# Optimization experiments

Hardware: AMD Instinct MI355X
Metric: run time of the kernel (lower is better)

The kernel has to match this reference:

```python
import jax, jax.numpy as jnp
import numpy as np
from functools import partial

SEQ, BATCH, IN, HID = 512, 128, 256, 1024


def setup_inputs() -> dict:
    key = jax.random.key(0)
    ks = jax.random.split(key, 8)
    std = 1.0 / np.sqrt(HID)
    u = lambda k, shape: jax.random.uniform(k, shape, jnp.float32, -std, std)
    return {
        "inp": jax.random.normal(ks[0], (SEQ, BATCH, IN), jnp.float32),
        "Wxh": u(ks[1], (4 * HID, IN)),
        "bxh": u(ks[2], (4 * HID,)),
        "Whh": u(ks[3], (4 * HID, HID)),
        "bhh": u(ks[4], (4 * HID,)),
        "Wout": u(ks[5], (IN, HID)),
        "bout": u(ks[6], (IN,)),
    }


def lstm_forward(inp, Wxh, bxh, Whh, bhh, Wout, bout):
    seq, batch, _ = inp.shape
    hid = Whh.shape[1]
    # Precompute input projection for all timesteps: [T, B, 4H]
    x_proj = jnp.einsum("tbi,gi->tbg", inp, Wxh) + bxh

    def step(carry, xp_t):
        h, c = carry
        gates = xp_t + h @ Whh.T + bhh            # [B, 4H]
        i, f, g, o = jnp.split(gates, 4, axis=-1)  # torch chunk order: i,f,g,o
        c = jax.nn.sigmoid(f) * c + jax.nn.sigmoid(i) * jnp.tanh(g)
        h = jax.nn.sigmoid(o) * jnp.tanh(c)
        return (h, c), h

    h0 = jnp.zeros((batch, hid), inp.dtype)
    c0 = jnp.zeros((batch, hid), inp.dtype)
    _, hs = jax.lax.scan(step, (h0, c0), x_proj)   # hs: [T, B, H]
    out = jnp.einsum("tbh,ih->tbi", hs, Wout) + bout
    return jax.nn.log_softmax(out, axis=-1)


def reference(inp, Wxh, bxh, Whh, bhh, Wout, bout):
    return lstm_forward(inp, Wxh, bxh, Whh, bhh, Wout, bout)
```

## Files before the change

### kernel.cpp

```cpp
#include <hip/hip_runtime.h>
#include <math.h>


#define TT  512
#define BB  128
#define NIN 256
#define NH  1024
#define G4  4096
#define KK  1280

typedef __bf16 bf16_t;
typedef bf16_t bf16x8 __attribute__((ext_vector_type(8)));
typedef float  f32x4  __attribute__((ext_vector_type(4)));


__global__ void conv_w_kernel(const float* __restrict__ Wxh,
                              const float* __restrict__ Whh,
                              bf16_t* __restrict__ Wc) {
  const int n = blockIdx.y;
  const int k = blockIdx.x * 256 + threadIdx.x;
  const int g = n & 3, j = n >> 2;
  float v = (k < NIN) ? Wxh[(size_t)(g * NH + j) * NIN + k]
                      : Whh[(size_t)(g * NH + j) * NH + (k - NIN)];
  Wc[(size_t)n * KK + k] = (bf16_t)v;
}

__global__ void conv_f2b_kernel(const float* __restrict__ src,
                                bf16_t* __restrict__ dst, int n4) {
  int i = blockIdx.x * 256 + threadIdx.x;
  if (i < n4) {
    float4 v = ((const float4*)src)[i];
    dst[i * 4 + 0] = (bf16_t)v.x;
    dst[i * 4 + 1] = (bf16_t)v.y;
    dst[i * 4 + 2] = (bf16_t)v.z;
    dst[i * 4 + 3] = (bf16_t)v.w;
  }
}

__global__ void prep_bias_kernel(const float* __restrict__ bxh,
                                 const float* __restrict__ bhh,
                                 float* __restrict__ bsum4) {
  int n = blockIdx.x * 256 + threadIdx.x;
  int g = n & 3, j = n >> 2;
  bsum4[n] = bxh[g * NH + j] + bhh[g * NH + j];
}


__global__ __launch_bounds__(256) void fused_step(
    int t,
    const bf16_t* __restrict__ x_bf,
    const bf16_t* __restrict__ Wc,
    const float*  __restrict__ bsum4,
    const bf16_t* __restrict__ h_cur,
    bf16_t*       __restrict__ h_next,
    float*        __restrict__ c,
    const bf16_t* __restrict__ WoutB,
    const float*  __restrict__ bout,
    float*        __restrict__ logits_w,
    const float*  __restrict__ logits_r,
    float*        __restrict__ out)
{
  const int blk  = blockIdx.x;
  const int tid  = threadIdx.x;
  const int lane = tid & 63;
  const int wv   = tid >> 6;
  const int l16  = lane & 15;
  const int lq   = lane >> 4;

  if (blk < 256) {
    if (t >= TT) return;
    __shared__ float gs[32][68];
    const int bm = (blk & 3) * 32;
    const int bn = (blk >> 2) * 64;
    const int wm = wv & 1, wn = wv >> 1;
    const int m0 = bm + wm * 16;
    const int n0 = bn + wn * 32;

    const bf16_t* ax  = x_bf + (size_t)t * BB * NIN + (size_t)(m0 + l16) * NIN + lq * 8;
    const bf16_t* ah  = h_cur + (size_t)(m0 + l16) * NH + lq * 8;
    const bf16_t* b0p = Wc + (size_t)(n0 + l16) * KK + lq * 8;
    const bf16_t* b1p = Wc + (size_t)(n0 + 16 + l16) * KK + lq * 8;

    f32x4 acc0 = {0.f, 0.f, 0.f, 0.f};
    f32x4 acc1 = {0.f, 0.f, 0.f, 0.f};

#pragma unroll 4
    for (int kk = 0; kk < NIN; kk += 32) {
      bf16x8 a  = *(const bf16x8*)(ax + kk);
      bf16x8 b0 = *(const bf16x8*)(b0p + kk);
      bf16x8 b1 = *(const bf16x8*)(b1p + kk);
      acc0 = __builtin_amdgcn_mfma_f32_16x16x32_bf16(a, b0, acc0, 0, 0, 0);
      acc1 = __builtin_amdgcn_mfma_f32_16x16x32_bf16(a, b1, acc1, 0, 0, 0);
    }
#pragma unroll 4
    for (int kk = 0; kk < NH; kk += 32) {
      bf16x8 a  = *(const bf16x8*)(ah + kk);
      bf16x8 b0 = *(const bf16x8*)(b0p + NIN + kk);
      bf16x8 b1 = *(const bf16x8*)(b1p + NIN + kk);
      acc0 = __builtin_amdgcn_mfma_f32_16x16x32_bf16(a, b0, acc0, 0, 0, 0);
      acc1 = __builtin_amdgcn_mfma_f32_16x16x32_bf16(a, b1, acc1, 0, 0, 0);
    }

#pragma unroll
    for (int r = 0; r < 4; ++r) {
      gs[wm * 16 + lq * 4 + r][wn * 32 + l16]      = acc0[r];
      gs[wm * 16 + lq * 4 + r][wn * 32 + 16 + l16] = acc1[r];
    }
    __syncthreads();

#pragma unroll
    for (int p = 0; p < 2; ++p) {
      const int u  = tid + p * 256;
      const int bl = u >> 4, jl = u & 15;
      float4 g4 = *(const float4*)&gs[bl][jl * 4];
      const int jg = (bn >> 2) + jl;
      float4 bs = ((const float4*)bsum4)[jg];
      const float gi = g4.x + bs.x;
      const float gf = g4.y + bs.y;
      const float gg = g4.z + bs.z;
      const float go = g4.w + bs.w;
      const float si = 1.f / (1.f + __expf(-gi));
      const float sf = 1.f / (1.f + __expf(-gf));
      const float so = 1.f / (1.f + __expf(-go));
      const float tg = tanhf(gg);
      const size_t idx = (size_t)(bm + bl) * NH + jg;
      const float cn = sf * c[idx] + si * tg;
      c[idx] = cn;
      h_next[idx] = (bf16_t)(so * tanhf(cn));
    }
  } else if (blk < 288) {
    if (t < 1 || t > TT) return;
    const int b2 = blk - 256;
    const int m0 = (b2 >> 2) * 16;
    const int n0 = (b2 & 3) * 64 + wv * 16;

    const bf16_t* ap = h_cur + (size_t)(m0 + l16) * NH + lq * 8;
    const bf16_t* bp = WoutB + (size_t)(n0 + l16) * NH + lq * 8;
    f32x4 acc = {0.f, 0.f, 0.f, 0.f};
#pragma unroll 4
    for (int kk = 0; kk < NH; kk += 32) {
      bf16x8 a = *(const bf16x8*)(ap + kk);
      bf16x8 b = *(const bf16x8*)(bp + kk);
      acc = __builtin_amdgcn_mfma_f32_16x16x32_bf16(a, b, acc, 0, 0, 0);
    }
    const int col = n0 + l16;
    const float bo = bout[col];
#pragma unroll
    for (int r = 0; r < 4; ++r)
      logits_w[(size_t)(m0 + lq * 4 + r) * NIN + col] = acc[r] + bo;
  } else {
    if (t < 2) return;
    __shared__ float red[2][4][4];
    const int b0 = (blk - 288) * 4;
    const float* lb = logits_r + (size_t)b0 * NIN;
    float v[4], mx[4], sm[4];
#pragma unroll
    for (int r = 0; r < 4; ++r) v[r] = lb[r * NIN + tid];
#pragma unroll
    for (int r = 0; r < 4; ++r) mx[r] = v[r];
#pragma unroll
    for (int off = 32; off > 0; off >>= 1)
#pragma unroll
      for (int r = 0; r < 4; ++r) mx[r] = fmaxf(mx[r], __shfl_xor(mx[r], off));
    if (lane == 0)
#pragma unroll
      for (int r = 0; r < 4; ++r) red[0][wv][r] = mx[r];
    __syncthreads();
#pragma unroll
    for (int r = 0; r < 4; ++r)
      mx[r] = fmaxf(fmaxf(red[0][0][r], red[0][1][r]),
                    fmaxf(red[0][2][r], red[0][3][r]));
#pragma unroll
    for (int r = 0; r < 4; ++r) sm[r] = __expf(v[r] - mx[r]);
#pragma unroll
    for (int off = 32; off > 0; off >>= 1)
#pragma unroll
      for (int r = 0; r < 4; ++r) sm[r] += __shfl_xor(sm[r], off);
    if (lane == 0)
#pragma unroll
      for (int r = 0; r < 4; ++r) red[1][wv][r] = sm[r];
    __syncthreads();
    float* ot = out + (size_t)(t - 2) * BB * NIN + (size_t)b0 * NIN;
#pragma unroll
    for (int r = 0; r < 4; ++r) {
      float S = red[1][0][r] + red[1][1][r] + red[1][2][r] + red[1][3][r];
      ot[r * NIN + tid] = v[r] - mx[r] - logf(S);
    }
  }
}


extern "C" void kernel_launch(void* const* d_in, const int* in_sizes, int n_in,
                              void* d_out, int out_size, void* d_ws, size_t ws_size,
                              hipStream_t stream) {
  const float* inp  = (const float*)d_in[0];
  const float* Wxh  = (const float*)d_in[1];
  const float* bxh  = (const float*)d_in[2];
  const float* Whh  = (const float*)d_in[3];
  const float* bhh  = (const float*)d_in[4];
  const float* Wout = (const float*)d_in[5];
  const float* bout = (const float*)d_in[6];
  float* out = (float*)d_out;

  char* p = (char*)d_ws;
  bf16_t* Wc    = (bf16_t*)p; p += (size_t)G4 * KK * 2;
  bf16_t* x_bf  = (bf16_t*)p; p += (size_t)TT * BB * NIN * 2;
  bf16_t* WoutB = (bf16_t*)p; p += (size_t)NIN * NH * 2;
  bf16_t* h0    = (bf16_t*)p; p += (size_t)BB * NH * 2;
  bf16_t* h1    = (bf16_t*)p; p += (size_t)BB * NH * 2;
  float*  cbuf  = (float*)p;  p += (size_t)BB * NH * 4;
  float*  bsum4 = (float*)p;  p += (size_t)G4 * 4;
  float*  lg0   = (float*)p;  p += (size_t)BB * NIN * 4;
  float*  lg1   = (float*)p;  p += (size_t)BB * NIN * 4;

  conv_w_kernel<<<dim3(KK / 256, G4), 256, 0, stream>>>(Wxh, Whh, Wc);
  conv_f2b_kernel<<<(TT * BB * NIN / 4 + 255) / 256, 256, 0, stream>>>(
      inp, x_bf, TT * BB * NIN / 4);
  conv_f2b_kernel<<<(NIN * NH / 4 + 255) / 256, 256, 0, stream>>>(
      Wout, WoutB, NIN * NH / 4);
  prep_bias_kernel<<<G4 / 256, 256, 0, stream>>>(bxh, bhh, bsum4);
  hipMemsetAsync(h0, 0, (size_t)BB * NH * 2, stream);
  hipMemsetAsync(cbuf, 0, (size_t)BB * NH * 4, stream);

  bf16_t* hb[2] = {h0, h1};
  float*  lg[2] = {lg0, lg1};
  for (int t = 0; t < TT + 2; ++t) {
    fused_step<<<320, 256, 0, stream>>>(
        t, x_bf, Wc, bsum4,
        hb[t & 1], hb[(t + 1) & 1], cbuf,
        WoutB, bout,
        lg[t & 1],
        lg[(t + 1) & 1],
        out);
  }
}
```

Measured before the change: 12.59 ms.

## Replace per-timestep launches with persistent cooperative kernel holding weights in registers

The 514 per-step kernel launches become one cooperative persistent kernel of 256 blocks that loops over timesteps and separates them with grid.sync(). Each wave loads its slice of the combined input and recurrent weights into 40 registers of bf16x8 once and reuses it for every step, so those weights are no longer re-read from memory each step. The cell state moves from a global buffer into per-thread registers. The costs are a grid-wide barrier per step, high register pressure from the resident weights, and the requirement that all 256 blocks be co-resident at once.

```diff
diff --git a/kernel.cpp b/kernel.cpp
--- a/kernel.cpp
+++ b/kernel.cpp
@@ -1,6 +1,9 @@
 #include <hip/hip_runtime.h>
+#include <hip/hip_cooperative_groups.h>
 #include <math.h>
 
+
+namespace cg = cooperative_groups;
 
 #define TT  512
 #define BB  128
@@ -12,6 +15,8 @@
 typedef __bf16 bf16_t;
 typedef bf16_t bf16x8 __attribute__((ext_vector_type(8)));
 typedef float  f32x4  __attribute__((ext_vector_type(4)));
+
+#define MFMA(a, b, c) __builtin_amdgcn_mfma_f32_16x16x32_bf16((a), (b), (c), 0, 0, 0)
 
 
 __global__ void conv_w_kernel(const float* __restrict__ Wxh,
@@ -46,20 +51,22 @@
 }
 
 
-__global__ __launch_bounds__(256) void fused_step(
-    int t,
+__global__ __launch_bounds__(256, 1) void lstm_persistent(
     const bf16_t* __restrict__ x_bf,
     const bf16_t* __restrict__ Wc,
     const float*  __restrict__ bsum4,
-    const bf16_t* __restrict__ h_cur,
-    bf16_t*       __restrict__ h_next,
-    float*        __restrict__ c,
+    bf16_t* __restrict__ hb0,
+    bf16_t* __restrict__ hb1,
+    float*  __restrict__ lgA,
+    float*  __restrict__ lgB,
     const bf16_t* __restrict__ WoutB,
     const float*  __restrict__ bout,
-    float*        __restrict__ logits_w,
-    const float*  __restrict__ logits_r,
-    float*        __restrict__ out)
+    float*  __restrict__ out)
 {
+  cg::grid_group grid = cg::this_grid();
+  __shared__ float gs[64 * 40];
+  __shared__ float red[2][4][4];
+
   const int blk  = blockIdx.x;
   const int tid  = threadIdx.x;
   const int lane = tid & 63;
@@ -67,125 +74,151 @@
   const int l16  = lane & 15;
   const int lq   = lane >> 4;
 
-  if (blk < 256) {
-    if (t >= TT) return;
-    __shared__ float gs[32][68];
-    const int bm = (blk & 3) * 32;
-    const int bn = (blk >> 2) * 64;
-    const int wm = wv & 1, wn = wv >> 1;
-    const int m0 = bm + wm * 16;
-    const int n0 = bn + wn * 32;
-
-    const bf16_t* ax  = x_bf + (size_t)t * BB * NIN + (size_t)(m0 + l16) * NIN + lq * 8;
-    const bf16_t* ah  = h_cur + (size_t)(m0 + l16) * NH + lq * 8;
-    const bf16_t* b0p = Wc + (size_t)(n0 + l16) * KK + lq * 8;
-    const bf16_t* b1p = Wc + (size_t)(n0 + 16 + l16) * KK + lq * 8;
-
-    f32x4 acc0 = {0.f, 0.f, 0.f, 0.f};
-    f32x4 acc1 = {0.f, 0.f, 0.f, 0.f};
-
-#pragma unroll 4
-    for (int kk = 0; kk < NIN; kk += 32) {
-      bf16x8 a  = *(const bf16x8*)(ax + kk);
-      bf16x8 b0 = *(const bf16x8*)(b0p + kk);
-      bf16x8 b1 = *(const bf16x8*)(b1p + kk);
-      acc0 = __builtin_amdgcn_mfma_f32_16x16x32_bf16(a, b0, acc0, 0, 0, 0);
-      acc1 = __builtin_amdgcn_mfma_f32_16x16x32_bf16(a, b1, acc1, 0, 0, 0);
+  const int mb = (blk & 1) * 64;
+  const int ns = blk >> 1;
+  const int wm = wv & 1, wn = wv >> 1;
+  const int m0 = mb + wm * 32;
+  const int n0 = ns * 32 + wn * 16;
+
+  bf16x8 w[40];
+  {
+    const bf16_t* wp = Wc + (size_t)(n0 + l16) * KK + lq * 8;
+#pragma unroll
+    for (int kk = 0; kk < 40; ++kk) w[kk] = *(const bf16x8*)(wp + kk * 32);
+  }
+
+  const int b_l = tid >> 3;
+  const int jl  = tid & 7;
+  const int jg  = ns * 8 + jl;
+  const float4 bs = ((const float4*)bsum4)[jg];
+  float c0 = 0.f, c1 = 0.f;
+
+  const int gw  = blk * 4 + wv;
+  const int bm0 = (gw >> 4) * 16;
+  const int bn0 = (gw & 15) * 16;
+  float boutv = 0.f;
+  const bf16_t* wob = WoutB;
+  if (blk < 32) {
+    boutv = bout[bn0 + l16];
+    wob = WoutB + (size_t)(bn0 + l16) * NH + lq * 8;
+  }
+
+  bf16_t* hb[2] = {hb0, hb1};
+  float*  lg[2] = {lgA, lgB};
+
+  for (int t = 0; t < TT + 2; ++t) {
+    const bf16_t* hc = hb[t & 1];
+    bf16_t*       hn = hb[(t + 1) & 1];
+
+    if (t < TT) {
+      f32x4 a00 = {0,0,0,0}, a01 = {0,0,0,0}, a10 = {0,0,0,0}, a11 = {0,0,0,0};
+      const bf16_t* ax = x_bf + (size_t)t * BB * NIN + (size_t)(m0 + l16) * NIN + lq * 8;
+#pragma unroll
+      for (int kk = 0; kk < 8; ++kk) {
+        bf16x8 r0 = *(const bf16x8*)(ax + kk * 32);
+        bf16x8 r1 = *(const bf16x8*)(ax + 16 * NIN + kk * 32);
+        a00 = MFMA(r0, w[kk], a00);
+        a10 = MFMA(r1, w[kk], a10);
+      }
+      const bf16_t* ah = hc + (size_t)(m0 + l16) * NH + lq * 8;
+#pragma unroll
+      for (int kk = 0; kk < 16; ++kk) {
+        bf16x8 r0 = *(const bf16x8*)(ah + kk * 32);
+        bf16x8 r1 = *(const bf16x8*)(ah + 16 * NH + kk * 32);
+        a00 = MFMA(r0, w[8 + kk], a00);
+        a10 = MFMA(r1, w[8 + kk], a10);
+      }
+#pragma unroll
+      for (int kk = 16; kk < 32; ++kk) {
+        bf16x8 r0 = *(const bf16x8*)(ah + kk * 32);
+        bf16x8 r1 = *(const bf16x8*)(ah + 16 * NH + kk * 32);
+        a01 = MFMA(r0, w[8 + kk], a01);
+        a11 = MFMA(r1, w[8 + kk], a11);
+      }
+      f32x4 acc0 = a00 + a01;
+      f32x4 acc1 = a10 + a11;
+
+#pragma unroll
+      for (int r = 0; r < 4; ++r) {
+        gs[(wm * 32 + lq * 4 + r) * 40 + wn * 16 + l16]      = acc0[r];
+        gs[(wm * 32 + 16 + lq * 4 + r) * 40 + wn * 16 + l16] = acc1[r];
+      }
+      __syncthreads();
+
+      {
+        float4 g0 = *(const float4*)&gs[b_l * 40 + jl * 4];
+        float4 g1 = *(const float4*)&gs[(b_l + 32) * 40 + jl * 4];
+        float gi = g0.x + bs.x, gf = g0.y + bs.y, gg = g0.z + bs.z, go = g0.w + bs.w;
+        float si = 1.f / (1.f + __expf(-gi));
+        float sf = 1.f / (1.f + __expf(-gf));
+        float so = 1.f / (1.f + __expf(-go));
+        c0 = sf * c0 + si * tanhf(gg);
+        hn[(size_t)(mb + b_l) * NH + jg] = (bf16_t)(so * tanhf(c0));
+
+        gi = g1.x + bs.x; gf = g1.y + bs.y; gg = g1.z + bs.z; go = g1.w + bs.w;
+        si = 1.f / (1.f + __expf(-gi));
+        sf = 1.f / (1.f + __expf(-gf));
+        so = 1.f / (1.f + __expf(-go));
+        c1 = sf * c1 + si * tanhf(gg);
+        hn[(size_t)(mb + b_l + 32) * NH + jg] = (bf16_t)(so * tanhf(c1));
+      }
     }
-#pragma unroll 4
-    for (int kk = 0; kk < NH; kk += 32) {
-      bf16x8 a  = *(const bf16x8*)(ah + kk);
-      bf16x8 b0 = *(const bf16x8*)(b0p + NIN + kk);
-      bf16x8 b1 = *(const bf16x8*)(b1p + NIN + kk);
-      acc0 = __builtin_amdgcn_mfma_f32_16x16x32_bf16(a, b0, acc0, 0, 0, 0);
-      acc1 = __builtin_amdgcn_mfma_f32_16x16x32_bf16(a, b1, acc1, 0, 0, 0);
+
+    if (blk < 32 && t >= 1 && t <= TT) {
+      const bf16_t* ap = hc + (size_t)(bm0 + l16) * NH + lq * 8;
+      f32x4 acc = {0,0,0,0};
+#pragma unroll
+      for (int kk = 0; kk < 32; ++kk) {
+        bf16x8 a = *(const bf16x8*)(ap + kk * 32);
+        bf16x8 b = *(const bf16x8*)(wob + kk * 32);
+        acc = MFMA(a, b, acc);
+      }
+      float* lw = lg[t & 1];
+#pragma unroll
+      for (int r = 0; r < 4; ++r)
+        lw[(size_t)(bm0 + lq * 4 + r) * NIN + bn0 + l16] = acc[r] + boutv;
     }
 
-#pragma unroll
-    for (int r = 0; r < 4; ++r) {
-      gs[wm * 16 + lq * 4 + r][wn * 32 + l16]      = acc0[r];
-      gs[wm * 16 + lq * 4 + r][wn * 32 + 16 + l16] = acc1[r];
+    if (blk >= 32 && blk < 64 && t >= 2) {
+      const float* lr = lg[(t + 1) & 1];
+      const int b0 = (blk - 32) * 4;
+      float v[4], mx[4], sm[4];
+#pragma unroll
+      for (int r = 0; r < 4; ++r) v[r] = lr[(size_t)(b0 + r) * NIN + tid];
+#pragma unroll
+      for (int r = 0; r < 4; ++r) mx[r] = v[r];
+#pragma unroll
+      for (int off = 32; off > 0; off >>= 1)
+#pragma unroll
+        for (int r = 0; r < 4; ++r) mx[r] = fmaxf(mx[r], __shfl_xor(mx[r], off));
+      if (lane == 0)
+#pragma unroll
+        for (int r = 0; r < 4; ++r) red[0][wv][r] = mx[r];
+      __syncthreads();
+#pragma unroll
+      for (int r = 0; r < 4; ++r)
+        mx[r] = fmaxf(fmaxf(red[0][0][r], red[0][1][r]),
+                      fmaxf(red[0][2][r], red[0][3][r]));
+#pragma unroll
+      for (int r = 0; r < 4; ++r) sm[r] = __expf(v[r] - mx[r]);
+#pragma unroll
+      for (int off = 32; off > 0; off >>= 1)
+#pragma unroll
+        for (int r = 0; r < 4; ++r) sm[r] += __shfl_xor(sm[r], off);
+      if (lane == 0)
+#pragma unroll
+        for (int r = 0; r < 4; ++r) red[1][wv][r] = sm[r];
+      __syncthreads();
+      float* ot = out + (size_t)(t - 2) * BB * NIN + (size_t)b0 * NIN;
+#pragma unroll
+      for (int r = 0; r < 4; ++r) {
+        float S = red[1][0][r] + red[1][1][r] + red[1][2][r] + red[1][3][r];
+        ot[(size_t)r * NIN + tid] = v[r] - mx[r] - logf(S);
+      }
+      __syncthreads();
     }
-    __syncthreads();
-
-#pragma unroll
-    for (int p = 0; p < 2; ++p) {
-      const int u  = tid + p * 256;
-      const int bl = u >> 4, jl = u & 15;
-      float4 g4 = *(const float4*)&gs[bl][jl * 4];
-      const int jg = (bn >> 2) + jl;
-      float4 bs = ((const float4*)bsum4)[jg];
-      const float gi = g4.x + bs.x;
-      const float gf = g4.y + bs.y;
-      const float gg = g4.z + bs.z;
-      const float go = g4.w + bs.w;
-      const float si = 1.f / (1.f + __expf(-gi));
-      const float sf = 1.f / (1.f + __expf(-gf));
-      const float so = 1.f / (1.f + __expf(-go));
-      const float tg = tanhf(gg);
-      const size_t idx = (size_t)(bm + bl) * NH + jg;
-      const float cn = sf * c[idx] + si * tg;
-      c[idx] = cn;
-      h_next[idx] = (bf16_t)(so * tanhf(cn));
-    }
-  } else if (blk < 288) {
-    if (t < 1 || t > TT) return;
-    const int b2 = blk - 256;
-    const int m0 = (b2 >> 2) * 16;
-    const int n0 = (b2 & 3) * 64 + wv * 16;
-
-    const bf16_t* ap = h_cur + (size_t)(m0 + l16) * NH + lq * 8;
-    const bf16_t* bp = WoutB + (size_t)(n0 + l16) * NH + lq * 8;
-    f32x4 acc = {0.f, 0.f, 0.f, 0.f};
-#pragma unroll 4
-    for (int kk = 0; kk < NH; kk += 32) {
-      bf16x8 a = *(const bf16x8*)(ap + kk);
-      bf16x8 b = *(const bf16x8*)(bp + kk);
-      acc = __builtin_amdgcn_mfma_f32_16x16x32_bf16(a, b, acc, 0, 0, 0);
-    }
-    const int col = n0 + l16;
-    const float bo = bout[col];
-#pragma unroll
-    for (int r = 0; r < 4; ++r)
-      logits_w[(size_t)(m0 + lq * 4 + r) * NIN + col] = acc[r] + bo;
-  } else {
-    if (t < 2) return;
-    __shared__ float red[2][4][4];
-    const int b0 = (blk - 288) * 4;
-    const float* lb = logits_r + (size_t)b0 * NIN;
-    float v[4], mx[4], sm[4];
-#pragma unroll
-    for (int r = 0; r < 4; ++r) v[r] = lb[r * NIN + tid];
-#pragma unroll
-    for (int r = 0; r < 4; ++r) mx[r] = v[r];
-#pragma unroll
-    for (int off = 32; off > 0; off >>= 1)
-#pragma unroll
-      for (int r = 0; r < 4; ++r) mx[r] = fmaxf(mx[r], __shfl_xor(mx[r], off));
-    if (lane == 0)
-#pragma unroll
-      for (int r = 0; r < 4; ++r) red[0][wv][r] = mx[r];
-    __syncthreads();
-#pragma unroll
-    for (int r = 0; r < 4; ++r)
-      mx[r] = fmaxf(fmaxf(red[0][0][r], red[0][1][r]),
-                    fmaxf(red[0][2][r], red[0][3][r]));
-#pragma unroll
-    for (int r = 0; r < 4; ++r) sm[r] = __expf(v[r] - mx[r]);
-#pragma unroll
-    for (int off = 32; off > 0; off >>= 1)
-#pragma unroll
-      for (int r = 0; r < 4; ++r) sm[r] += __shfl_xor(sm[r], off);
-    if (lane == 0)
-#pragma unroll
-      for (int r = 0; r < 4; ++r) red[1][wv][r] = sm[r];
-    __syncthreads();
-    float* ot = out + (size_t)(t - 2) * BB * NIN + (size_t)b0 * NIN;
-#pragma unroll
-    for (int r = 0; r < 4; ++r) {
-      float S = red[1][0][r] + red[1][1][r] + red[1][2][r] + red[1][3][r];
-      ot[r * NIN + tid] = v[r] - mx[r] - logf(S);
-    }
+
+    grid.sync();
   }
 }
 
@@ -200,7 +233,7 @@
   const float* bhh  = (const float*)d_in[4];
   const float* Wout = (const float*)d_in[5];
   const float* bout = (const float*)d_in[6];
-  float* out = (float*)d_out;
+  float* outp = (float*)d_out;
 
   char* p = (char*)d_ws;
   bf16_t* Wc    = (bf16_t*)p; p += (size_t)G4 * KK * 2;
@@ -208,7 +241,6 @@
   bf16_t* WoutB = (bf16_t*)p; p += (size_t)NIN * NH * 2;
   bf16_t* h0    = (bf16_t*)p; p += (size_t)BB * NH * 2;
   bf16_t* h1    = (bf16_t*)p; p += (size_t)BB * NH * 2;
-  float*  cbuf  = (float*)p;  p += (size_t)BB * NH * 4;
   float*  bsum4 = (float*)p;  p += (size_t)G4 * 4;
   float*  lg0   = (float*)p;  p += (size_t)BB * NIN * 4;
   float*  lg1   = (float*)p;  p += (size_t)BB * NIN * 4;
@@ -220,17 +252,8 @@
       Wout, WoutB, NIN * NH / 4);
   prep_bias_kernel<<<G4 / 256, 256, 0, stream>>>(bxh, bhh, bsum4);
   hipMemsetAsync(h0, 0, (size_t)BB * NH * 2, stream);
-  hipMemsetAsync(cbuf, 0, (size_t)BB * NH * 4, stream);
-
-  bf16_t* hb[2] = {h0, h1};
-  float*  lg[2] = {lg0, lg1};
-  for (int t = 0; t < TT + 2; ++t) {
-    fused_step<<<320, 256, 0, stream>>>(
-        t, x_bf, Wc, bsum4,
-        hb[t & 1], hb[(t + 1) & 1], cbuf,
-        WoutB, bout,
-        lg[t & 1],
-        lg[(t + 1) & 1],
-        out);
-  }
-}
+
+  void* args[] = {&x_bf, &Wc, &bsum4, &h0, &h1, &lg0, &lg1, &WoutB, &bout, &outp};
+  hipLaunchCooperativeKernel((void*)lstm_persistent, dim3(256), dim3(256),
+                             args, 0, stream);
+}
```

Result: slower. 24.19 ms (+92.1%).

## Enlarge LSTM step tiles to 64x64 with 2x2 MFMA register blocking

Applied to the files above, without the earlier changes.

The recurrent GEMM block tile grows from 32x64 to 64x64 per workgroup, and each wave now computes a 32x32 sub-tile with four accumulators. This lets each A and B fragment load feed two MFMAs, which halves the redundant global and L2 loads of the weight matrix across batch tiles. The GEMM block count drops from 256 to 128 and the launch grid from 320 to 192. The output projection is remapped so each wave owns a 16x16 tile across 32 blocks. The trade-off is fewer workgroups per step, which lowers parallelism on a GPU with many CUs in exchange for better operand reuse.

```diff
diff --git a/kernel.cpp b/kernel.cpp
--- a/kernel.cpp
+++ b/kernel.cpp
@@ -12,6 +12,8 @@
 typedef __bf16 bf16_t;
 typedef bf16_t bf16x8 __attribute__((ext_vector_type(8)));
 typedef float  f32x4  __attribute__((ext_vector_type(4)));
+
+#define MFMA(a, b, c) __builtin_amdgcn_mfma_f32_16x16x32_bf16((a), (b), (c), 0, 0, 0)
 
 
 __global__ void conv_w_kernel(const float* __restrict__ Wxh,
@@ -67,54 +69,60 @@
   const int l16  = lane & 15;
   const int lq   = lane >> 4;
 
-  if (blk < 256) {
+  if (blk < 128) {
     if (t >= TT) return;
-    __shared__ float gs[32][68];
-    const int bm = (blk & 3) * 32;
-    const int bn = (blk >> 2) * 64;
+    __shared__ float gs[64 * 68];
+
+    const int mb    = (blk & 1) * 64;
+    const int ns    = blk >> 1;
+    const int nbase = ns * 64;
     const int wm = wv & 1, wn = wv >> 1;
-    const int m0 = bm + wm * 16;
-    const int n0 = bn + wn * 32;
+    const int m0 = mb + wm * 32;
+    const int n0 = nbase + wn * 32;
 
     const bf16_t* ax  = x_bf + (size_t)t * BB * NIN + (size_t)(m0 + l16) * NIN + lq * 8;
     const bf16_t* ah  = h_cur + (size_t)(m0 + l16) * NH + lq * 8;
     const bf16_t* b0p = Wc + (size_t)(n0 + l16) * KK + lq * 8;
     const bf16_t* b1p = Wc + (size_t)(n0 + 16 + l16) * KK + lq * 8;
 
-    f32x4 acc0 = {0.f, 0.f, 0.f, 0.f};
-    f32x4 acc1 = {0.f, 0.f, 0.f, 0.f};
-
-#pragma unroll 4
-    for (int kk = 0; kk < NIN; kk += 32) {
-      bf16x8 a  = *(const bf16x8*)(ax + kk);
-      bf16x8 b0 = *(const bf16x8*)(b0p + kk);
-      bf16x8 b1 = *(const bf16x8*)(b1p + kk);
-      acc0 = __builtin_amdgcn_mfma_f32_16x16x32_bf16(a, b0, acc0, 0, 0, 0);
-      acc1 = __builtin_amdgcn_mfma_f32_16x16x32_bf16(a, b1, acc1, 0, 0, 0);
-    }
-#pragma unroll 4
-    for (int kk = 0; kk < NH; kk += 32) {
-      bf16x8 a  = *(const bf16x8*)(ah + kk);
-      bf16x8 b0 = *(const bf16x8*)(b0p + NIN + kk);
-      bf16x8 b1 = *(const bf16x8*)(b1p + NIN + kk);
-      acc0 = __builtin_amdgcn_mfma_f32_16x16x32_bf16(a, b0, acc0, 0, 0, 0);
-      acc1 = __builtin_amdgcn_mfma_f32_16x16x32_bf16(a, b1, acc1, 0, 0, 0);
+    f32x4 a00 = {0,0,0,0}, a01 = {0,0,0,0}, a10 = {0,0,0,0}, a11 = {0,0,0,0};
+
+#pragma unroll
+    for (int kk = 0; kk < 8; ++kk) {
+      bf16x8 r0 = *(const bf16x8*)(ax + kk * 32);
+      bf16x8 r1 = *(const bf16x8*)(ax + 16 * NIN + kk * 32);
+      bf16x8 b0 = *(const bf16x8*)(b0p + kk * 32);
+      bf16x8 b1 = *(const bf16x8*)(b1p + kk * 32);
+      a00 = MFMA(r0, b0, a00); a01 = MFMA(r0, b1, a01);
+      a10 = MFMA(r1, b0, a10); a11 = MFMA(r1, b1, a11);
+    }
+#pragma unroll 8
+    for (int kk = 0; kk < 32; ++kk) {
+      bf16x8 r0 = *(const bf16x8*)(ah + kk * 32);
+      bf16x8 r1 = *(const bf16x8*)(ah + 16 * NH + kk * 32);
+      bf16x8 b0 = *(const bf16x8*)(b0p + NIN + kk * 32);
+      bf16x8 b1 = *(const bf16x8*)(b1p + NIN + kk * 32);
+      a00 = MFMA(r0, b0, a00); a01 = MFMA(r0, b1, a01);
+      a10 = MFMA(r1, b0, a10); a11 = MFMA(r1, b1, a11);
     }
 
 #pragma unroll
     for (int r = 0; r < 4; ++r) {
-      gs[wm * 16 + lq * 4 + r][wn * 32 + l16]      = acc0[r];
-      gs[wm * 16 + lq * 4 + r][wn * 32 + 16 + l16] = acc1[r];
+      const int rr0 = wm * 32 + lq * 4 + r;
+      gs[rr0 * 68 + wn * 32 + l16]             = a00[r];
+      gs[rr0 * 68 + wn * 32 + 16 + l16]        = a01[r];
+      gs[(rr0 + 16) * 68 + wn * 32 + l16]      = a10[r];
+      gs[(rr0 + 16) * 68 + wn * 32 + 16 + l16] = a11[r];
     }
     __syncthreads();
 
-#pragma unroll
-    for (int p = 0; p < 2; ++p) {
-      const int u  = tid + p * 256;
-      const int bl = u >> 4, jl = u & 15;
-      float4 g4 = *(const float4*)&gs[bl][jl * 4];
-      const int jg = (bn >> 2) + jl;
-      float4 bs = ((const float4*)bsum4)[jg];
+    const int b_l = tid >> 2;
+#pragma unroll
+    for (int p = 0; p < 4; ++p) {
+      const int jl = (tid & 3) + p * 4;
+      const int j  = ns * 16 + jl;
+      float4 g4 = *(const float4*)&gs[b_l * 68 + jl * 4];
+      float4 bs = ((const float4*)bsum4)[j];
       const float gi = g4.x + bs.x;
       const float gf = g4.y + bs.y;
       const float gg = g4.z + bs.z;
@@ -122,40 +130,37 @@
       const float si = 1.f / (1.f + __expf(-gi));
       const float sf = 1.f / (1.f + __expf(-gf));
       const float so = 1.f / (1.f + __expf(-go));
-      const float tg = tanhf(gg);
-      const size_t idx = (size_t)(bm + bl) * NH + jg;
-      const float cn = sf * c[idx] + si * tg;
+      const size_t idx = (size_t)(mb + b_l) * NH + j;
+      const float cn = sf * c[idx] + si * tanhf(gg);
       c[idx] = cn;
       h_next[idx] = (bf16_t)(so * tanhf(cn));
     }
-  } else if (blk < 288) {
+  } else if (blk < 160) {
     if (t < 1 || t > TT) return;
-    const int b2 = blk - 256;
-    const int m0 = (b2 >> 2) * 16;
-    const int n0 = (b2 & 3) * 64 + wv * 16;
-
-    const bf16_t* ap = h_cur + (size_t)(m0 + l16) * NH + lq * 8;
-    const bf16_t* bp = WoutB + (size_t)(n0 + l16) * NH + lq * 8;
-    f32x4 acc = {0.f, 0.f, 0.f, 0.f};
-#pragma unroll 4
-    for (int kk = 0; kk < NH; kk += 32) {
-      bf16x8 a = *(const bf16x8*)(ap + kk);
-      bf16x8 b = *(const bf16x8*)(bp + kk);
-      acc = __builtin_amdgcn_mfma_f32_16x16x32_bf16(a, b, acc, 0, 0, 0);
-    }
-    const int col = n0 + l16;
-    const float bo = bout[col];
+    const int gw  = (blk - 128) * 4 + wv;
+    const int bm0 = (gw >> 4) * 16;
+    const int bn0 = (gw & 15) * 16;
+
+    const bf16_t* ap = h_cur + (size_t)(bm0 + l16) * NH + lq * 8;
+    const bf16_t* bp = WoutB + (size_t)(bn0 + l16) * NH + lq * 8;
+    f32x4 acc = {0,0,0,0};
+#pragma unroll 8
+    for (int kk = 0; kk < 32; ++kk) {
+      bf16x8 a = *(const bf16x8*)(ap + kk * 32);
+      bf16x8 b = *(const bf16x8*)(bp + kk * 32);
+      acc = MFMA(a, b, acc);
+    }
+    const float bo = bout[bn0 + l16];
 #pragma unroll
     for (int r = 0; r < 4; ++r)
-      logits_w[(size_t)(m0 + lq * 4 + r) * NIN + col] = acc[r] + bo;
+      logits_w[(size_t)(bm0 + lq * 4 + r) * NIN + bn0 + l16] = acc[r] + bo;
   } else {
     if (t < 2) return;
     __shared__ float red[2][4][4];
-    const int b0 = (blk - 288) * 4;
-    const float* lb = logits_r + (size_t)b0 * NIN;
+    const int b0 = (blk - 160) * 4;
     float v[4], mx[4], sm[4];
 #pragma unroll
-    for (int r = 0; r < 4; ++r) v[r] = lb[r * NIN + tid];
+    for (int r = 0; r < 4; ++r) v[r] = logits_r[(size_t)(b0 + r) * NIN + tid];
 #pragma unroll
     for (int r = 0; r < 4; ++r) mx[r] = v[r];
 #pragma unroll
@@ -184,7 +189,7 @@
 #pragma unroll
     for (int r = 0; r < 4; ++r) {
       float S = red[1][0][r] + red[1][1][r] + red[1][2][r] + red[1][3][r];
-      ot[r * NIN + tid] = v[r] - mx[r] - logf(S);
+      ot[(size_t)r * NIN + tid] = v[r] - mx[r] - logf(S);
     }
   }
 }
@@ -225,7 +230,7 @@
   bf16_t* hb[2] = {h0, h1};
   float*  lg[2] = {lg0, lg1};
   for (int t = 0; t < TT + 2; ++t) {
-    fused_step<<<320, 256, 0, stream>>>(
+    fused_step<<<192, 256, 0, stream>>>(
         t, x_bf, Wc, bsum4,
         hb[t & 1], hb[(t + 1) & 1], cbuf,
         WoutB, bout,
```

Measured after the change: 11.15 ms. -11.4%, faster.
